# Kernel tuning notes

Hardware: AMD Instinct MI355X
Metric: run time of the kernel (lower is better)

## Reference

```python
import jax, jax.numpy as jnp
from jax import lax
import numpy as np


def gen_position(p, pos_decay=1.0):
    # Fixed relative-position bias: (9, p*p), neighbor order di*3+dj
    ar = jnp.arange(p, dtype=jnp.float32)
    right = jnp.broadcast_to(jnp.exp(-ar / (p / pos_decay))[None, :], (p, p))  # decays along width
    down = right.T                                                             # decays along height
    i, j = jnp.meshgrid(ar, ar, indexing='ij')
    br = jnp.exp(-(i + j) / (p / pos_decay))
    ones = jnp.ones((p, p), jnp.float32)
    merge = jnp.stack([
        jnp.rot90(br, 2), down[::-1, :], jnp.rot90(br, 1),
        right[:, ::-1], ones, right,
        jnp.rot90(br, 3), down, br,
    ], axis=0)
    return merge.reshape(9, -1)


def attention_conv(x, w_qkv, b_qkv, head_w, window_size, num_heads):
    b, c, h, w = x.shape
    p = window_size // 3
    pad_h = (p * (1 + h // p) - h) % p
    pad_w = (p * (1 + w // p) - w) % p
    xp = jnp.pad(x, ((0, 0), (0, 0), (p + pad_h, p), (p + pad_w, p)), mode='reflect')
    Hp, Wp = xp.shape[2], xp.shape[3]
    nH, nW = Hp // p - 2, Wp // p - 2  # == number of unfold windows (stride p, size 3p)
    # Non-overlapping p x p tiles; each window = 3x3 grid of adjacent tiles.
    tiles = xp.reshape(b, c, nH + 2, p, nW + 2, p).transpose(0, 2, 4, 1, 3, 5)  # [b,nH+2,nW+2,c,p,p]
    neigh = jnp.stack([tiles[:, di:di + nH, dj:dj + nW]
                       for di in range(3) for dj in range(3)], axis=3)  # [b,nH,nW,9,c,p,p]
    L = c * p * p
    pp = p * p
    xw = neigh.reshape(b * nH * nW, 9, L)
    qkv = xw @ w_qkv.T + b_qkv                                  # [N,9,nh*3*L]
    qkv = qkv.reshape(-1, 9, num_heads, 3, c, pp).transpose(0, 2, 4, 3, 1, 5)  # [N,nh,C,3,9,pp]
    q, k, v = qkv[:, :, :, 0], qkv[:, :, :, 1], qkv[:, :, :, 2]  # each [N,nh,C,9,pp]
    bias = gen_position(p)                                       # [9,pp]
    core_q = q[:, :, :, 4, :]                                    # center patch query [N,nh,C,pp]
    score = jnp.einsum('nhcp,nhckp->nhck', core_q, k * bias) / jnp.sqrt(jnp.float32(L))
    attn = jax.nn.softmax(score, axis=-1)                        # over 9 neighbors
    out = jnp.einsum('nhck,nhckp->nhcp', attn, v).reshape(-1, num_heads, L)
    out = jnp.einsum('h,nhd->nd', head_w[0], out)                # head mixing [N,L]
    out = out.reshape(b, nH, nW, c, p, p).transpose(0, 3, 1, 4, 2, 5).reshape(b, c, nH * p, nW * p)
    return out[:, :, pad_h:, pad_w:]


def setup_inputs() -> dict:
    key = jax.random.key(0)
    ks = jax.random.split(key, 8)
    B, C, H, W = 4, 3, 256, 256
    x = jax.random.uniform(ks[0], (B, C, H, W), dtype=jnp.float32)
    # conv3: window 3, p=1, heads 6, L=3 ; conv6: window 6, p=2, heads 4, L=12 ; conv9: window 9, p=3, heads 2, L=27
    w3_qkv = jax.random.normal(ks[1], (6 * 3 * 3, 3), jnp.float32) * 0.2
    b3_qkv = jnp.zeros((6 * 3 * 3,), jnp.float32)
    hw3 = jnp.full((1, 6), 1.0 / 6.0, jnp.float32)
    w6_qkv = jax.random.normal(ks[2], (4 * 3 * 12, 12), jnp.float32) * 0.1
    b6_qkv = jnp.zeros((4 * 3 * 12,), jnp.float32)
    hw6 = jnp.full((1, 4), 1.0 / 4.0, jnp.float32)
    w9_qkv = jax.random.normal(ks[3], (2 * 3 * 27, 27), jnp.float32) * 0.07
    b9_qkv = jnp.zeros((2 * 3 * 27,), jnp.float32)
    hw9 = jnp.full((1, 2), 1.0 / 2.0, jnp.float32)
    conv0_w = jax.random.normal(ks[4], (3, 9, 5, 5), jnp.float32) * 0.05
    conv0_b = jnp.zeros((3,), jnp.float32)
    return {"x": x, "w3_qkv": w3_qkv, "b3_qkv": b3_qkv, "hw3": hw3,
            "w6_qkv": w6_qkv, "b6_qkv": b6_qkv, "hw6": hw6,
            "w9_qkv": w9_qkv, "b9_qkv": b9_qkv, "hw9": hw9,
            "conv0_w": conv0_w, "conv0_b": conv0_b}


def reference(x, w3_qkv, b3_qkv, hw3, w6_qkv, b6_qkv, hw6,
              w9_qkv, b9_qkv, hw9, conv0_w, conv0_b):
    b, c, h, w = x.shape
    # global prior: softmax over size-1 dim (== ones), then global max pool
    gavg = jnp.mean((1.0 - x).reshape(b, c, -1), axis=-1, keepdims=True)       # [b,c,1]
    x_g = jax.nn.softmax(gavg, axis=-1)[..., None]                             # [b,c,1,1]
    x_g = jnp.max((x * x_g).reshape(b, 1, -1), axis=-1, keepdims=True)[..., None]  # [b,1,1,1]
    x3 = attention_conv(x,  w3_qkv, b3_qkv, hw3, 3, 6)
    x6 = attention_conv(x3, w6_qkv, b6_qkv, hw6, 6, 4)
    x9 = attention_conv(x6, w9_qkv, b9_qkv, hw9, 9, 2)
    cat = jnp.concatenate([x9, x6, x3], axis=1)                                # [b,9,h,w]
    x0 = jax.nn.relu(lax.conv_general_dilated(cat, conv0_w, (1, 1), ((2, 2), (2, 2)),
                                              dimension_numbers=('NCHW', 'OIHW', 'NCHW'))
                     + conv0_b[None, :, None, None])
    return jax.nn.relu(x * x0 + (x_g - x0))
```

## Files before the change

### kernel.cpp

```cpp
#include <hip/hip_runtime.h>
#include <hip/hip_fp16.h>
#include <math.h>

__device__ __forceinline__ int refl256(int t) {
    t = t < 0 ? -t : t;
    return t > 255 ? 510 - t : t;
}

__device__ __forceinline__ void unpack4h(uint2 u, float* g4) {
    __half2 h01 = *(__half2*)&u.x, h23 = *(__half2*)&u.y;
    g4[0] = __low2float(h01); g4[1] = __high2float(h01);
    g4[2] = __low2float(h23); g4[3] = __high2float(h23);
}

__global__ __launch_bounds__(256)
void attn_p1v2(const float* __restrict__ x, const float* __restrict__ w,
               const float* __restrict__ bq, const float* __restrict__ hw,
               float* __restrict__ out, float* __restrict__ pmax)
{
    const int slot = threadIdx.x;
    const int hg = __builtin_amdgcn_readfirstlane((int)threadIdx.y);
    int t2 = blockIdx.x * 128 + slot;
    int xx = t2 & 255, yp = (t2 >> 8) & 127, bb = t2 >> 15;
    int y0 = yp * 2;
    const float* xb = x + bb * 196608;
    int rs[4], cs[3];
#pragma unroll
    for (int dr = 0; dr < 4; ++dr) rs[dr] = refl256(y0 + dr - 1) << 8;
#pragma unroll
    for (int dc = 0; dc < 3; ++dc) cs[dc] = refl256(xx + dc - 1);
    float xw[4][3][3];
#pragma unroll
    for (int dr = 0; dr < 4; ++dr)
#pragma unroll
        for (int dc = 0; dc < 3; ++dc)
#pragma unroll
            for (int c = 0; c < 3; ++c)
                xw[dr][dc][c] = xb[c * 65536 + rs[dr] + cs[dc]];

    {
        float bm = 0.f;
#pragma unroll
        for (int c = 0; c < 3; ++c)
            bm = fmaxf(bm, fmaxf(xw[1][1][c], xw[2][1][c]));
#pragma unroll
        for (int off = 32; off > 0; off >>= 1)
            bm = fmaxf(bm, __shfl_down(bm, off, 64));
        __shared__ float sm[4];
        int flat = threadIdx.y * 128 + slot;
        if ((flat & 63) == 0) sm[flat >> 6] = bm;
        __syncthreads();
        if (flat == 0)
            pmax[blockIdx.x] = fmaxf(fmaxf(sm[0], sm[1]), fmaxf(sm[2], sm[3]));
    }

    float ov0[3] = {0.f, 0.f, 0.f}, ov1[3] = {0.f, 0.f, 0.f};
    const float scl = 0.57735026919f;
#pragma unroll 1
    for (int hi = 0; hi < 3; ++hi) {
        int h = hg * 3 + hi;
        float hwh = hw[h];
#pragma unroll
        for (int cc = 0; cc < 3; ++cc) {
            int oq = 9 * h + cc, ok = oq + 3, oV = oq + 6;
            float wq0 = w[oq * 3], wq1 = w[oq * 3 + 1], wq2 = w[oq * 3 + 2];
            float wk0 = w[ok * 3], wk1 = w[ok * 3 + 1], wk2 = w[ok * 3 + 2];
            float wv0 = w[oV * 3], wv1 = w[oV * 3 + 1], wv2 = w[oV * 3 + 2];
            float bk = bq[ok], bv = bq[oV];
            float kp[12], vp[12];
#pragma unroll
            for (int pos = 0; pos < 12; ++pos) {
                const float* xv = xw[pos / 3][pos % 3];
                kp[pos] = fmaf(xv[0], wk0, fmaf(xv[1], wk1, fmaf(xv[2], wk2, bk)));
                vp[pos] = fmaf(xv[0], wv0, fmaf(xv[1], wv1, fmaf(xv[2], wv2, bv)));
            }
            float q0 = fmaf(xw[1][1][0], wq0, fmaf(xw[1][1][1], wq1, fmaf(xw[1][1][2], wq2, bq[oq]))) * scl;
            float q1 = fmaf(xw[2][1][0], wq0, fmaf(xw[2][1][1], wq1, fmaf(xw[2][1][2], wq2, bq[oq]))) * scl;
            float se0 = 0.f, ac0 = 0.f, se1 = 0.f, ac1 = 0.f;
#pragma unroll
            for (int j = 0; j < 9; ++j) {
                float e0 = __expf(q0 * kp[j]);
                se0 += e0; ac0 = fmaf(e0, vp[j], ac0);
                float e1 = __expf(q1 * kp[3 + j]);
                se1 += e1; ac1 = fmaf(e1, vp[3 + j], ac1);
            }
            ov0[cc] = fmaf(hwh, ac0 / se0, ov0[cc]);
            ov1[cc] = fmaf(hwh, ac1 / se1, ov1[cc]);
        }
    }
    __shared__ float s_part[128][6];
    if (hg == 1) {
#pragma unroll
        for (int cc = 0; cc < 3; ++cc) {
            s_part[slot][cc] = ov0[cc];
            s_part[slot][3 + cc] = ov1[cc];
        }
    }
    __syncthreads();
    if (hg == 0) {
        int pix = (y0 << 8) + xx;
        float* ob = out + bb * 196608;
#pragma unroll
        for (int cc = 0; cc < 3; ++cc) {
            ob[cc * 65536 + pix] = ov0[cc] + s_part[slot][cc];
            ob[cc * 65536 + pix + 256] = ov1[cc] + s_part[slot][3 + cc];
        }
    }
}

template<int P, int NH, int NWIN, int OFS, int GSU, int NCH>
__global__ __launch_bounds__(64 * NCH)
void proj3_pk(const float* __restrict__ x, const float* __restrict__ w,
              const float* __restrict__ bq, uint2* __restrict__ kv)
{
    constexpr int PP = P * P, L = 3 * PP, NO = NH * 9 * PP, NG = NO / GSU;
    constexpr int CPG = NG / NCH;
    constexpr int NT = NWIN + 2, T4 = 4 * NT * NT;
    int t = blockIdx.x * 64 + threadIdx.x;
    if (t >= T4) return;
    const int chunk = __builtin_amdgcn_readfirstlane((int)threadIdx.y);
    int bb = t / (NT * NT), rr = t - bb * NT * NT;
    int ty = rr / NT, tx = rr - ty * NT;
    const float* xb = x + bb * 196608;
    float xw[L];
#pragma unroll
    for (int i = 0; i < P; ++i) {
        int pr = refl256(ty * P + i - OFS) << 8;
#pragma unroll
        for (int j = 0; j < P; ++j) {
            int pc = refl256(tx * P + j - OFS);
#pragma unroll
            for (int c = 0; c < 3; ++c)
                xw[c * PP + i * P + j] = xb[c * 65536 + pr + pc];
        }
    }
    uint2* dst = kv + t + (size_t)chunk * CPG * T4;
#pragma unroll 1
    for (int g = 0; g < CPG; ++g) {
        int go = (chunk * CPG + g) * GSU;
        float acc[GSU];
#pragma unroll
        for (int e = 0; e < GSU; ++e) acc[e] = bq[go + e];
#pragma unroll
        for (int l = 0; l < L; ++l) {
            float xv = xw[l];
#pragma unroll
            for (int e = 0; e < GSU; ++e)
                acc[e] = fmaf(xv, w[(go + e) * L + l], acc[e]);
        }
        __half2 a01 = __floats2half2_rn(acc[0], acc[1]);
        __half2 a23 = __floats2half2_rn(acc[2], (GSU == 4) ? acc[GSU - 1] : 0.f);
        uint2 o;
        o.x = *(unsigned*)&a01;
        o.y = *(unsigned*)&a23;
        dst[(size_t)g * T4] = o;
    }
}

template<int P, int NH, int NWIN, int OFS, int GSU, int HPT>
__global__ __launch_bounds__(256)
void attn3_pk(const uint2* __restrict__ kv, const float* __restrict__ hw,
              float* __restrict__ out)
{
    constexpr int PP = P * P, NT = NWIN + 2, T4 = 4 * NT * NT, PAD = OFS - P;
    constexpr int NGP = (PP + GSU - 1) / GSU;
    constexpr float SCL = (P == 2) ? 0.28867513459481287f : 0.19245008972987526f;
    constexpr float DD  = (P == 2) ? 0.6065306597126334f : 0.7165313105737893f;
    float dpw[2 * P - 1];
    dpw[0] = 1.f;
#pragma unroll
    for (int k = 1; k < 2 * P - 1; ++k) dpw[k] = dpw[k - 1] * DD;

    const int slot = threadIdx.x;
    const int hg = __builtin_amdgcn_readfirstlane((int)threadIdx.y);
    int wlin = blockIdx.x * 128 + slot;
    const bool active = wlin < 4 * NWIN * NWIN;
    int wsafe = active ? wlin : 0;
    int c = blockIdx.y;
    int bb = wsafe / (NWIN * NWIN); int rr = wsafe - bb * (NWIN * NWIN);
    int yy = rr / NWIN, xx = rr - yy * NWIN;
    int tbase = bb * NT * NT + yy * NT + xx;
    int tn[9];
#pragma unroll
    for (int di = 0; di < 3; ++di)
#pragma unroll
        for (int dj = 0; dj < 3; ++dj) tn[di * 3 + dj] = tbase + di * NT + dj;
    float oa[PP];
#pragma unroll
    for (int e = 0; e < PP; ++e) oa[e] = 0.f;
#pragma unroll 1
    for (int hi = 0; hi < HPT; ++hi) {
        int h = hg * HPT + hi;
        int oq = ((h * 3 + 0) * 3 + c) * PP;
        int ok = ((h * 3 + 1) * 3 + c) * PP;
        int ov = ((h * 3 + 2) * 3 + c) * PP;
        int gq = oq / GSU, gk = ok / GSU, gv = ov / GSU;
        float q[PP];
#pragma unroll
        for (int u = 0; u < NGP; ++u) {
            float g4[4];
            unpack4h(kv[(size_t)(gq + u) * T4 + tn[4]], g4);
#pragma unroll
            for (int e = 0; e < GSU; ++e) q[u * GSU + e] = g4[e];
        }
        float sc[9];
#pragma unroll
        for (int j = 0; j < 9; ++j) {
            int di = j / 3, dj = j - di * 3;
            float s = 0.f;
#pragma unroll
            for (int u = 0; u < NGP; ++u) {
                float g4[4];
                unpack4h(kv[(size_t)(gk + u) * T4 + tn[j]], g4);
#pragma unroll
                for (int e = 0; e < GSU; ++e) {
                    int Pp = u * GSU + e;
                    int i = Pp / P, jj = Pp - i * P;
                    int er = (di == 0) ? (P - 1 - i) : (di == 2 ? i : 0);
                    int ec = (dj == 0) ? (P - 1 - jj) : (dj == 2 ? jj : 0);
                    s = fmaf(q[Pp] * g4[e], dpw[er + ec], s);
                }
            }
            sc[j] = s * SCL;
        }
        float se = 0.f;
#pragma unroll
        for (int j = 0; j < 9; ++j) { sc[j] = __expf(sc[j]); se += sc[j]; }
        float tmp[PP];
#pragma unroll
        for (int e = 0; e < PP; ++e) tmp[e] = 0.f;
#pragma unroll
        for (int j = 0; j < 9; ++j) {
#pragma unroll
            for (int u = 0; u < NGP; ++u) {
                float g4[4];
                unpack4h(kv[(size_t)(gv + u) * T4 + tn[j]], g4);
#pragma unroll
                for (int e = 0; e < GSU; ++e)
                    tmp[u * GSU + e] = fmaf(sc[j], g4[e], tmp[u * GSU + e]);
            }
        }
        float f = hw[h] / se;
#pragma unroll
        for (int e = 0; e < PP; ++e) oa[e] = fmaf(f, tmp[e], oa[e]);
    }
    __shared__ float s_part[128][PP];
    if (hg == 1) {
#pragma unroll
        for (int e = 0; e < PP; ++e) s_part[slot][e] = oa[e];
    }
    __syncthreads();
    if (hg == 0 && active) {
        float* ob = out + (bb * 3 + c) * 65536;
#pragma unroll
        for (int i = 0; i < P; ++i) {
            int r = yy * P + i - PAD;
            if (PAD && r < 0) continue;
#pragma unroll
            for (int jj = 0; jj < P; ++jj) {
                int col = xx * P + jj - PAD;
                if (PAD && col < 0) continue;
                int e = i * P + jj;
                ob[(r << 8) + col] = oa[e] + s_part[slot][e];
            }
        }
    }
}

__global__ __launch_bounds__(384)
void conv_finalv3(const float* __restrict__ x, const float* __restrict__ x9,
                  const float* __restrict__ x6, const float* __restrict__ x3,
                  const float* __restrict__ cw, const float* __restrict__ cb,
                  const float* __restrict__ pmax, float* __restrict__ out)
{
    const int slot = threadIdx.x;
    const int src = __builtin_amdgcn_readfirstlane((int)threadIdx.y);
    int bb = blockIdx.x >> 8;
    __shared__ float s_g;
    {
        int flat = threadIdx.y * 128 + slot;
        if (flat < 64) {
            const float* pm = pmax + bb * 256 + flat * 4;
            float v = fmaxf(fmaxf(pm[0], pm[1]), fmaxf(pm[2], pm[3]));
#pragma unroll
            for (int off = 32; off > 0; off >>= 1)
                v = fmaxf(v, __shfl_down(v, off, 64));
            if (flat == 0) s_g = v;
        }
    }
    int pair = (blockIdx.x & 255) * 128 + slot;
    int xp = (pair & 127) << 1, r = pair >> 7;
    float a[3][2];
#pragma unroll
    for (int oc = 0; oc < 3; ++oc) { a[oc][0] = 0.f; a[oc][1] = 0.f; }
    const float* bp = (src == 0 ? x9 : (src == 1 ? x6 : x3)) + bb * 196608;
#pragma unroll 1
    for (int c2 = 0; c2 < 3; ++c2) {
        const float* pl = bp + c2 * 65536;
        const float* wp = cw + (src * 3 + c2) * 25;
#pragma unroll
        for (int ky = 0; ky < 5; ++ky) {
            int rr = r + ky - 2;
            if ((unsigned)rr >= 256u) continue;
            const float* row = pl + (rr << 8);
            float2 va = (xp >= 2) ? *(const float2*)(row + xp - 2)
                                  : make_float2(0.f, 0.f);
            float2 vb = *(const float2*)(row + xp);
            float2 vc = (xp + 2 < 256) ? *(const float2*)(row + xp + 2)
                                       : make_float2(0.f, 0.f);
            float cv[6] = {va.x, va.y, vb.x, vb.y, vc.x, vc.y};
#pragma unroll
            for (int kx = 0; kx < 5; ++kx) {
                float w0 = wp[ky * 5 + kx];
                float w1 = wp[225 + ky * 5 + kx];
                float w2 = wp[450 + ky * 5 + kx];
                float v0 = cv[kx], v1 = cv[kx + 1];
                a[0][0] = fmaf(v0, w0, a[0][0]); a[0][1] = fmaf(v1, w0, a[0][1]);
                a[1][0] = fmaf(v0, w1, a[1][0]); a[1][1] = fmaf(v1, w1, a[1][1]);
                a[2][0] = fmaf(v0, w2, a[2][0]); a[2][1] = fmaf(v1, w2, a[2][1]);
            }
        }
    }
    __shared__ float s_part[2][128][6];
    if (src > 0) {
#pragma unroll
        for (int oc = 0; oc < 3; ++oc) {
            s_part[src - 1][slot][oc * 2]     = a[oc][0];
            s_part[src - 1][slot][oc * 2 + 1] = a[oc][1];
        }
    }
    __syncthreads();
    if (src == 0) {
        float g = s_g;
        int pix = (r << 8) + xp;
        const float* xb = x + bb * 196608;
        float* ob = out + bb * 196608;
#pragma unroll
        for (int oc = 0; oc < 3; ++oc) {
            float a0 = a[oc][0] + s_part[0][slot][oc * 2] + s_part[1][slot][oc * 2] + cb[oc];
            float a1 = a[oc][1] + s_part[0][slot][oc * 2 + 1] + s_part[1][slot][oc * 2 + 1] + cb[oc];
            float2 xv = *(const float2*)(xb + oc * 65536 + pix);
            float2 o2;
            float x0;
            x0 = fmaxf(a0, 0.f); o2.x = fmaxf(xv.x * x0 + g - x0, 0.f);
            x0 = fmaxf(a1, 0.f); o2.y = fmaxf(xv.y * x0 + g - x0, 0.f);
            *(float2*)(ob + oc * 65536 + pix) = o2;
        }
    }
}

extern "C" void kernel_launch(void* const* d_in, const int* in_sizes, int n_in,
                              void* d_out, int out_size, void* d_ws, size_t ws_size,
                              hipStream_t stream)
{
    const float* x   = (const float*)d_in[0];
    const float* w3  = (const float*)d_in[1];
    const float* b3  = (const float*)d_in[2];
    const float* hw3 = (const float*)d_in[3];
    const float* w6  = (const float*)d_in[4];
    const float* b6  = (const float*)d_in[5];
    const float* hw6 = (const float*)d_in[6];
    const float* w9  = (const float*)d_in[7];
    const float* b9  = (const float*)d_in[8];
    const float* hw9 = (const float*)d_in[9];
    const float* cw  = (const float*)d_in[10];
    const float* cb  = (const float*)d_in[11];

    float* ws   = (float*)d_ws;
    float* x3b  = ws;
    float* x6b  = ws + 786432;
    float* x9b  = ws + 1572864;
    float* pmax = ws + 2359296;
    uint2* kvb  = (uint2*)(ws + 2360320);
    float* out  = (float*)d_out;

    attn_p1v2<<<1024, dim3(128, 2), 0, stream>>>(x, w3, b3, hw3, x3b, pmax);

    proj3_pk<2, 4, 128, 2, 4, 6><<<1057, dim3(64, 6), 0, stream>>>(x3b, w6, b6, kvb);
    attn3_pk<2, 4, 128, 2, 4, 2><<<dim3(512, 3), dim3(128, 2), 0, stream>>>(kvb, hw6, x6b);
    proj3_pk<3, 2, 86, 5, 3, 9><<<484, dim3(64, 9), 0, stream>>>(x6b, w9, b9, kvb);
    attn3_pk<3, 2, 86, 5, 3, 1><<<dim3(232, 3), dim3(128, 2), 0, stream>>>(kvb, hw9, x9b);

    conv_finalv3<<<1024, dim3(128, 3), 0, stream>>>(x, x9b, x6b, x3b, cw, cb, pmax, out);
}
```

Measured before the change: 155.5 us.

## Interleave K/V storage, fuse single-pass softmax, and process 2x2 pixel quads in stage one

The first attention stage now has each thread handle a 2x2 pixel quad instead of a 2x1 column pair. Neighbour K/V projections are then shared across four outputs, half as many blocks are launched, and stores use float2. In the later stages, K and V for the same group are packed together into one uint4, and the scores, exp and V accumulation happen in a single pass over the 9 neighbours. This removes a separate V-load sweep, and the pmax reduction in the final kernel is adjusted to the halved partial count. The cost is higher register pressure, since each thread now holds 16 neighbour positions and extra V registers.

```diff
diff --git a/kernel.cpp b/kernel.cpp
--- a/kernel.cpp
+++ b/kernel.cpp
@@ -12,28 +12,37 @@
     g4[0] = __low2float(h01); g4[1] = __high2float(h01);
     g4[2] = __low2float(h23); g4[3] = __high2float(h23);
 }
+__device__ __forceinline__ void unpack8h(uint4 u, float* k4, float* v4) {
+    __half2 a = *(__half2*)&u.x, b = *(__half2*)&u.y;
+    __half2 c = *(__half2*)&u.z, d = *(__half2*)&u.w;
+    k4[0] = __low2float(a); k4[1] = __high2float(a);
+    k4[2] = __low2float(b); k4[3] = __high2float(b);
+    v4[0] = __low2float(c); v4[1] = __high2float(c);
+    v4[2] = __low2float(d); v4[3] = __high2float(d);
+}
 
 __global__ __launch_bounds__(256)
-void attn_p1v2(const float* __restrict__ x, const float* __restrict__ w,
-               const float* __restrict__ bq, const float* __restrict__ hw,
-               float* __restrict__ out, float* __restrict__ pmax)
+void attn_p1q(const float* __restrict__ x, const float* __restrict__ w,
+              const float* __restrict__ bq, const float* __restrict__ hw,
+              float* __restrict__ out, float* __restrict__ pmax)
 {
     const int slot = threadIdx.x;
     const int hg = __builtin_amdgcn_readfirstlane((int)threadIdx.y);
     int t2 = blockIdx.x * 128 + slot;
-    int xx = t2 & 255, yp = (t2 >> 8) & 127, bb = t2 >> 15;
-    int y0 = yp * 2;
+    int qx = t2 & 127, qy = (t2 >> 7) & 127, bb = t2 >> 14;
+    int x0 = qx * 2, y0 = qy * 2;
     const float* xb = x + bb * 196608;
-    int rs[4], cs[3];
-#pragma unroll
-    for (int dr = 0; dr < 4; ++dr) rs[dr] = refl256(y0 + dr - 1) << 8;
-#pragma unroll
-    for (int dc = 0; dc < 3; ++dc) cs[dc] = refl256(xx + dc - 1);
-    float xw[4][3][3];
+    int rs[4], cs[4];
+#pragma unroll
+    for (int d = 0; d < 4; ++d) {
+        rs[d] = refl256(y0 + d - 1) << 8;
+        cs[d] = refl256(x0 + d - 1);
+    }
+    float xw[4][4][3];
 #pragma unroll
     for (int dr = 0; dr < 4; ++dr)
 #pragma unroll
-        for (int dc = 0; dc < 3; ++dc)
+        for (int dc = 0; dc < 4; ++dc)
 #pragma unroll
             for (int c = 0; c < 3; ++c)
                 xw[dr][dc][c] = xb[c * 65536 + rs[dr] + cs[dc]];
@@ -41,8 +50,10 @@
     {
         float bm = 0.f;
 #pragma unroll
-        for (int c = 0; c < 3; ++c)
-            bm = fmaxf(bm, fmaxf(xw[1][1][c], xw[2][1][c]));
+        for (int c = 0; c < 3; ++c) {
+            bm = fmaxf(bm, fmaxf(xw[1][1][c], xw[1][2][c]));
+            bm = fmaxf(bm, fmaxf(xw[2][1][c], xw[2][2][c]));
+        }
 #pragma unroll
         for (int off = 32; off > 0; off >>= 1)
             bm = fmaxf(bm, __shfl_down(bm, off, 64));
@@ -54,7 +65,13 @@
             pmax[blockIdx.x] = fmaxf(fmaxf(sm[0], sm[1]), fmaxf(sm[2], sm[3]));
     }
 
-    float ov0[3] = {0.f, 0.f, 0.f}, ov1[3] = {0.f, 0.f, 0.f};
+    float ov[2][2][3];
+#pragma unroll
+    for (int py = 0; py < 2; ++py)
+#pragma unroll
+        for (int px = 0; px < 2; ++px)
+#pragma unroll
+            for (int c = 0; c < 3; ++c) ov[py][px][c] = 0.f;
     const float scl = 0.57735026919f;
 #pragma unroll 1
     for (int hi = 0; hi < 3; ++hi) {
@@ -66,59 +83,70 @@
             float wq0 = w[oq * 3], wq1 = w[oq * 3 + 1], wq2 = w[oq * 3 + 2];
             float wk0 = w[ok * 3], wk1 = w[ok * 3 + 1], wk2 = w[ok * 3 + 2];
             float wv0 = w[oV * 3], wv1 = w[oV * 3 + 1], wv2 = w[oV * 3 + 2];
-            float bk = bq[ok], bv = bq[oV];
-            float kp[12], vp[12];
-#pragma unroll
-            for (int pos = 0; pos < 12; ++pos) {
-                const float* xv = xw[pos / 3][pos % 3];
+            float bqq = bq[oq], bk = bq[ok], bv = bq[oV];
+            float kp[16], vp[16];
+#pragma unroll
+            for (int pos = 0; pos < 16; ++pos) {
+                const float* xv = xw[pos >> 2][pos & 3];
                 kp[pos] = fmaf(xv[0], wk0, fmaf(xv[1], wk1, fmaf(xv[2], wk2, bk)));
                 vp[pos] = fmaf(xv[0], wv0, fmaf(xv[1], wv1, fmaf(xv[2], wv2, bv)));
             }
-            float q0 = fmaf(xw[1][1][0], wq0, fmaf(xw[1][1][1], wq1, fmaf(xw[1][1][2], wq2, bq[oq]))) * scl;
-            float q1 = fmaf(xw[2][1][0], wq0, fmaf(xw[2][1][1], wq1, fmaf(xw[2][1][2], wq2, bq[oq]))) * scl;
-            float se0 = 0.f, ac0 = 0.f, se1 = 0.f, ac1 = 0.f;
-#pragma unroll
-            for (int j = 0; j < 9; ++j) {
-                float e0 = __expf(q0 * kp[j]);
-                se0 += e0; ac0 = fmaf(e0, vp[j], ac0);
-                float e1 = __expf(q1 * kp[3 + j]);
-                se1 += e1; ac1 = fmaf(e1, vp[3 + j], ac1);
-            }
-            ov0[cc] = fmaf(hwh, ac0 / se0, ov0[cc]);
-            ov1[cc] = fmaf(hwh, ac1 / se1, ov1[cc]);
-        }
-    }
-    __shared__ float s_part[128][6];
+#pragma unroll
+            for (int py = 0; py < 2; ++py)
+#pragma unroll
+                for (int px = 0; px < 2; ++px) {
+                    const float* xc = xw[1 + py][1 + px];
+                    float q = fmaf(xc[0], wq0, fmaf(xc[1], wq1, fmaf(xc[2], wq2, bqq))) * scl;
+                    float se = 0.f, ac = 0.f;
+#pragma unroll
+                    for (int dr = 0; dr < 3; ++dr)
+#pragma unroll
+                        for (int dc = 0; dc < 3; ++dc) {
+                            int pos = (py + dr) * 4 + (px + dc);
+                            float e0 = __expf(q * kp[pos]);
+                            se += e0; ac = fmaf(e0, vp[pos], ac);
+                        }
+                    ov[py][px][cc] = fmaf(hwh, ac / se, ov[py][px][cc]);
+                }
+        }
+    }
+    __shared__ float s_part[128][12];
     if (hg == 1) {
 #pragma unroll
-        for (int cc = 0; cc < 3; ++cc) {
-            s_part[slot][cc] = ov0[cc];
-            s_part[slot][3 + cc] = ov1[cc];
-        }
+        for (int py = 0; py < 2; ++py)
+#pragma unroll
+            for (int px = 0; px < 2; ++px)
+#pragma unroll
+                for (int cc = 0; cc < 3; ++cc)
+                    s_part[slot][(py * 2 + px) * 3 + cc] = ov[py][px][cc];
     }
     __syncthreads();
     if (hg == 0) {
-        int pix = (y0 << 8) + xx;
         float* ob = out + bb * 196608;
 #pragma unroll
-        for (int cc = 0; cc < 3; ++cc) {
-            ob[cc * 65536 + pix] = ov0[cc] + s_part[slot][cc];
-            ob[cc * 65536 + pix + 256] = ov1[cc] + s_part[slot][3 + cc];
-        }
+        for (int cc = 0; cc < 3; ++cc)
+#pragma unroll
+            for (int py = 0; py < 2; ++py) {
+                float2 o2;
+                o2.x = ov[py][0][cc] + s_part[slot][(py * 2 + 0) * 3 + cc];
+                o2.y = ov[py][1][cc] + s_part[slot][(py * 2 + 1) * 3 + cc];
+                *(float2*)(ob + cc * 65536 + ((y0 + py) << 8) + x0) = o2;
+            }
     }
 }
 
 template<int P, int NH, int NWIN, int OFS, int GSU, int NCH>
 __global__ __launch_bounds__(64 * NCH)
-void proj3_pk(const float* __restrict__ x, const float* __restrict__ w,
-              const float* __restrict__ bq, uint2* __restrict__ kv)
+void proj4_pk(const float* __restrict__ x, const float* __restrict__ w,
+              const float* __restrict__ bq,
+              uint2* __restrict__ kvq, uint4* __restrict__ kvv)
 {
-    constexpr int PP = P * P, L = 3 * PP, NO = NH * 9 * PP, NG = NO / GSU;
-    constexpr int CPG = NG / NCH;
+    constexpr int PP = P * P, L = 3 * PP, NGP = PP / GSU;
+    constexpr int QS = NH * 3 * NGP, TOT = 2 * QS;
     constexpr int NT = NWIN + 2, T4 = 4 * NT * NT;
     int t = blockIdx.x * 64 + threadIdx.x;
     if (t >= T4) return;
-    const int chunk = __builtin_amdgcn_readfirstlane((int)threadIdx.y);
+    const int wvi = __builtin_amdgcn_readfirstlane((int)threadIdx.y);
     int bb = t / (NT * NT), rr = t - bb * NT * NT;
     int ty = rr / NT, tx = rr - ty * NT;
     const float* xb = x + bb * 196608;
@@ -134,36 +162,69 @@
                 xw[c * PP + i * P + j] = xb[c * 65536 + pr + pc];
         }
     }
-    uint2* dst = kv + t + (size_t)chunk * CPG * T4;
 #pragma unroll 1
-    for (int g = 0; g < CPG; ++g) {
-        int go = (chunk * CPG + g) * GSU;
-        float acc[GSU];
-#pragma unroll
-        for (int e = 0; e < GSU; ++e) acc[e] = bq[go + e];
-#pragma unroll
-        for (int l = 0; l < L; ++l) {
-            float xv = xw[l];
-#pragma unroll
-            for (int e = 0; e < GSU; ++e)
-                acc[e] = fmaf(xv, w[(go + e) * L + l], acc[e]);
-        }
-        __half2 a01 = __floats2half2_rn(acc[0], acc[1]);
-        __half2 a23 = __floats2half2_rn(acc[2], (GSU == 4) ? acc[GSU - 1] : 0.f);
-        uint2 o;
-        o.x = *(unsigned*)&a01;
-        o.y = *(unsigned*)&a23;
-        dst[(size_t)g * T4] = o;
+    for (int s = wvi; s < TOT; s += NCH) {
+        int sq = (s < QS) ? s : s - QS;
+        int h = sq / (3 * NGP);
+        int rem = sq - h * (3 * NGP);
+        int c = rem / NGP, u = rem - c * NGP;
+        if (s < QS) {
+            int ob = ((h * 3 + 0) * 3 + c) * PP + u * GSU;
+            float acc[GSU];
+#pragma unroll
+            for (int e = 0; e < GSU; ++e) acc[e] = bq[ob + e];
+#pragma unroll
+            for (int l = 0; l < L; ++l) {
+                float xv = xw[l];
+#pragma unroll
+                for (int e = 0; e < GSU; ++e)
+                    acc[e] = fmaf(xv, w[(ob + e) * L + l], acc[e]);
+            }
+            __half2 a01 = __floats2half2_rn(acc[0], acc[1]);
+            __half2 a23 = __floats2half2_rn(GSU > 2 ? acc[2] : 0.f,
+                                            GSU > 3 ? acc[GSU - 1] : 0.f);
+            uint2 o;
+            o.x = *(unsigned*)&a01;
+            o.y = *(unsigned*)&a23;
+            kvq[(size_t)sq * T4 + t] = o;
+        } else {
+            int okb = ((h * 3 + 1) * 3 + c) * PP + u * GSU;
+            int ovb = ((h * 3 + 2) * 3 + c) * PP + u * GSU;
+            float ak[GSU], av[GSU];
+#pragma unroll
+            for (int e = 0; e < GSU; ++e) { ak[e] = bq[okb + e]; av[e] = bq[ovb + e]; }
+#pragma unroll
+            for (int l = 0; l < L; ++l) {
+                float xv = xw[l];
+#pragma unroll
+                for (int e = 0; e < GSU; ++e) {
+                    ak[e] = fmaf(xv, w[(okb + e) * L + l], ak[e]);
+                    av[e] = fmaf(xv, w[(ovb + e) * L + l], av[e]);
+                }
+            }
+            __half2 k01 = __floats2half2_rn(ak[0], ak[1]);
+            __half2 k23 = __floats2half2_rn(GSU > 2 ? ak[2] : 0.f,
+                                            GSU > 3 ? ak[GSU - 1] : 0.f);
+            __half2 v01 = __floats2half2_rn(av[0], av[1]);
+            __half2 v23 = __floats2half2_rn(GSU > 2 ? av[2] : 0.f,
+                                            GSU > 3 ? av[GSU - 1] : 0.f);
+            uint4 o;
+            o.x = *(unsigned*)&k01;
+            o.y = *(unsigned*)&k23;
+            o.z = *(unsigned*)&v01;
+            o.w = *(unsigned*)&v23;
+            kvv[(size_t)sq * T4 + t] = o;
+        }
     }
 }
 
 template<int P, int NH, int NWIN, int OFS, int GSU, int HPT>
 __global__ __launch_bounds__(256)
-void attn3_pk(const uint2* __restrict__ kv, const float* __restrict__ hw,
-              float* __restrict__ out)
+void attn4_pk(const uint2* __restrict__ kvq, const uint4* __restrict__ kvv,
+              const float* __restrict__ hw, float* __restrict__ out)
 {
-    constexpr int PP = P * P, NT = NWIN + 2, T4 = 4 * NT * NT, PAD = OFS - P;
-    constexpr int NGP = (PP + GSU - 1) / GSU;
+    constexpr int PP = P * P, NGP = PP / GSU;
+    constexpr int NT = NWIN + 2, T4 = 4 * NT * NT, PAD = OFS - P;
     constexpr float SCL = (P == 2) ? 0.28867513459481287f : 0.19245008972987526f;
     constexpr float DD  = (P == 2) ? 0.6065306597126334f : 0.7165313105737893f;
     float dpw[2 * P - 1];
@@ -191,54 +252,42 @@
 #pragma unroll 1
     for (int hi = 0; hi < HPT; ++hi) {
         int h = hg * HPT + hi;
-        int oq = ((h * 3 + 0) * 3 + c) * PP;
-        int ok = ((h * 3 + 1) * 3 + c) * PP;
-        int ov = ((h * 3 + 2) * 3 + c) * PP;
-        int gq = oq / GSU, gk = ok / GSU, gv = ov / GSU;
+        int sb = (h * 3 + c) * NGP;
         float q[PP];
 #pragma unroll
         for (int u = 0; u < NGP; ++u) {
             float g4[4];
-            unpack4h(kv[(size_t)(gq + u) * T4 + tn[4]], g4);
+            unpack4h(kvq[(size_t)(sb + u) * T4 + tn[4]], g4);
 #pragma unroll
             for (int e = 0; e < GSU; ++e) q[u * GSU + e] = g4[e];
         }
-        float sc[9];
+        float se = 0.f;
+        float tmp[PP];
+#pragma unroll
+        for (int e = 0; e < PP; ++e) tmp[e] = 0.f;
 #pragma unroll
         for (int j = 0; j < 9; ++j) {
             int di = j / 3, dj = j - di * 3;
+            float vreg[PP];
             float s = 0.f;
 #pragma unroll
             for (int u = 0; u < NGP; ++u) {
-                float g4[4];
-                unpack4h(kv[(size_t)(gk + u) * T4 + tn[j]], g4);
+                float k4[4], v4[4];
+                unpack8h(kvv[(size_t)(sb + u) * T4 + tn[j]], k4, v4);
 #pragma unroll
                 for (int e = 0; e < GSU; ++e) {
                     int Pp = u * GSU + e;
                     int i = Pp / P, jj = Pp - i * P;
                     int er = (di == 0) ? (P - 1 - i) : (di == 2 ? i : 0);
                     int ec = (dj == 0) ? (P - 1 - jj) : (dj == 2 ? jj : 0);
-                    s = fmaf(q[Pp] * g4[e], dpw[er + ec], s);
+                    s = fmaf(q[Pp] * k4[e], dpw[er + ec], s);
+                    vreg[Pp] = v4[e];
                 }
             }
-            sc[j] = s * SCL;
-        }
-        float se = 0.f;
-#pragma unroll
-        for (int j = 0; j < 9; ++j) { sc[j] = __expf(sc[j]); se += sc[j]; }
-        float tmp[PP];
-#pragma unroll
-        for (int e = 0; e < PP; ++e) tmp[e] = 0.f;
-#pragma unroll
-        for (int j = 0; j < 9; ++j) {
-#pragma unroll
-            for (int u = 0; u < NGP; ++u) {
-                float g4[4];
-                unpack4h(kv[(size_t)(gv + u) * T4 + tn[j]], g4);
-#pragma unroll
-                for (int e = 0; e < GSU; ++e)
-                    tmp[u * GSU + e] = fmaf(sc[j], g4[e], tmp[u * GSU + e]);
-            }
+            float e2 = __expf(s * SCL);
+            se += e2;
+#pragma unroll
+            for (int e = 0; e < PP; ++e) tmp[e] = fmaf(e2, vreg[e], tmp[e]);
         }
         float f = hw[h] / se;
 #pragma unroll
@@ -279,11 +328,11 @@
     __shared__ float s_g;
     {
         int flat = threadIdx.y * 128 + slot;
-        if (flat < 64) {
-            const float* pm = pmax + bb * 256 + flat * 4;
+        if (flat < 32) {
+            const float* pm = pmax + bb * 128 + flat * 4;
             float v = fmaxf(fmaxf(pm[0], pm[1]), fmaxf(pm[2], pm[3]));
 #pragma unroll
-            for (int off = 32; off > 0; off >>= 1)
+            for (int off = 16; off > 0; off >>= 1)
                 v = fmaxf(v, __shfl_down(v, off, 64));
             if (flat == 0) s_g = v;
         }
@@ -371,15 +420,16 @@
     float* x6b  = ws + 786432;
     float* x9b  = ws + 1572864;
     float* pmax = ws + 2359296;
-    uint2* kvb  = (uint2*)(ws + 2360320);
+    uint2* kvq  = (uint2*)(ws + 2360320);
+    uint4* kvv  = (uint4*)(ws + 3982720);
     float* out  = (float*)d_out;
 
-    attn_p1v2<<<1024, dim3(128, 2), 0, stream>>>(x, w3, b3, hw3, x3b, pmax);
-
-    proj3_pk<2, 4, 128, 2, 4, 6><<<1057, dim3(64, 6), 0, stream>>>(x3b, w6, b6, kvb);
-    attn3_pk<2, 4, 128, 2, 4, 2><<<dim3(512, 3), dim3(128, 2), 0, stream>>>(kvb, hw6, x6b);
-    proj3_pk<3, 2, 86, 5, 3, 9><<<484, dim3(64, 9), 0, stream>>>(x6b, w9, b9, kvb);
-    attn3_pk<3, 2, 86, 5, 3, 1><<<dim3(232, 3), dim3(128, 2), 0, stream>>>(kvb, hw9, x9b);
+    attn_p1q<<<512, dim3(128, 2), 0, stream>>>(x, w3, b3, hw3, x3b, pmax);
+
+    proj4_pk<2, 4, 128, 2, 4, 6><<<1057, dim3(64, 6), 0, stream>>>(x3b, w6, b6, kvq, kvv);
+    attn4_pk<2, 4, 128, 2, 4, 2><<<dim3(512, 3), dim3(128, 2), 0, stream>>>(kvq, kvv, hw6, x6b);
+    proj4_pk<3, 2, 86, 5, 3, 9><<<484, dim3(64, 9), 0, stream>>>(x6b, w9, b9, kvq, kvv);
+    attn4_pk<3, 2, 86, 5, 3, 1><<<dim3(232, 3), dim3(128, 2), 0, stream>>>(kvq, kvv, hw9, x9b);
 
     conv_finalv3<<<1024, dim3(128, 3), 0, stream>>>(x, x9b, x6b, x3b, cw, cb, pmax, out);
 }
```

Measured after the change: 151.4 us. 2.7% less time.
